# Kernel tuning notes

Hardware: AMD Instinct MI355X
Metric: run time of the kernel (lower is better)

The kernel has to match this reference:

```python
import jax, jax.numpy as jnp
import numpy as np

N_EMBD = 768
N_HEAD = 12
HEAD_DIM = N_EMBD // N_HEAD


def setup_inputs() -> dict:
    key = jax.random.key(0)
    k0, k1, k2, k3, k4 = jax.random.split(key, 5)
    B, T, C = 2, 4096, N_EMBD
    x = jax.random.normal(k0, (B, T, C), dtype=jnp.float32)
    # c_attn: Linear(C, 3C); c_proj: Linear(C, C). torch Linear: y = x @ W.T + b
    s = 1.0 / np.sqrt(C)
    W_attn = jax.random.uniform(k1, (3 * C, C), dtype=jnp.float32, minval=-s, maxval=s)
    b_attn = jax.random.uniform(k2, (3 * C,), dtype=jnp.float32, minval=-s, maxval=s)
    W_proj = jax.random.uniform(k3, (C, C), dtype=jnp.float32, minval=-s, maxval=s)
    b_proj = jax.random.uniform(k4, (C,), dtype=jnp.float32, minval=-s, maxval=s)
    return {"x": x, "W_attn": W_attn, "b_attn": b_attn, "W_proj": W_proj, "b_proj": b_proj}


def reference(x, W_attn, b_attn, W_proj, b_proj):
    B, T, C = x.shape
    H, D = N_HEAD, HEAD_DIM
    qkv = x @ W_attn.T + b_attn                      # [B,T,3C]
    q, k, v = jnp.split(qkv, 3, axis=-1)
    # [B,T,C] -> [B,H,T,D]
    q = q.reshape(B, T, H, D).transpose(0, 2, 1, 3)
    k = k.reshape(B, T, H, D).transpose(0, 2, 1, 3)
    v = v.reshape(B, T, H, D).transpose(0, 2, 1, 3)
    scale = 1.0 / jnp.sqrt(jnp.asarray(D, dtype=x.dtype))
    att = jnp.einsum('bhqd,bhkd->bhqk', q, k) * scale  # [B,H,T,T]
    att = jax.nn.softmax(att, axis=-1)
    y = jnp.einsum('bhqk,bhkd->bhqd', att, v)          # [B,H,T,D]
    y = y.transpose(0, 2, 1, 3).reshape(B, T, C)
    return y @ W_proj.T + b_proj
```

## Files before the change

### kernel.cpp

```cpp
#include <hip/hip_runtime.h>
#include <stdint.h>
#include <stddef.h>

typedef __bf16 bf16_t;
typedef bf16_t bf16x4 __attribute__((ext_vector_type(4)));
typedef bf16_t bf16x8 __attribute__((ext_vector_type(8)));
typedef float  f32x4  __attribute__((ext_vector_type(4)));

#define MFMA16(a, b, c) __builtin_amdgcn_mfma_f32_16x16x32_bf16(a, b, c, 0, 0, 0)

__device__ __forceinline__ void gload_lds16(const bf16_t* g, bf16_t* l) {
    __builtin_amdgcn_global_load_lds(
        (const __attribute__((address_space(1))) void*)g,
        (__attribute__((address_space(3))) void*)l,
        16, 0, 0);
}

__global__ void cvt_f32_bf16(const float* __restrict__ in, bf16_t* __restrict__ out, int n4) {
    int i = blockIdx.x * blockDim.x + threadIdx.x;
    if (i >= n4) return;
    float4 f = ((const float4*)in)[i];
    bf16x4 o = { (bf16_t)f.x, (bf16_t)f.y, (bf16_t)f.z, (bf16_t)f.w };
    ((bf16x4*)out)[i] = o;
}

template <int KDIM>
__device__ __forceinline__ void gemm_mainloop(
    const bf16_t* __restrict__ A, const bf16_t* __restrict__ Bt,
    bf16_t* As, bf16_t* Bs, int m0, int n0, int wave, int lane, f32x4 acc[4][4])
{
    const int quad = lane >> 4, l15 = lane & 15;
    const int wm = ((wave >> 1) << 6), wn = ((wave & 1) << 6);

    const int srow = (wave << 4) + (lane >> 2);
    const int sw   = (((lane & 3) ^ ((srow >> 1) & 3)) << 3);
    const bf16_t* gA = A  + (size_t)(m0 + srow) * KDIM + sw;
    const bf16_t* gB = Bt + (size_t)(n0 + srow) * KDIM + sw;
    bf16_t* lA0 = As + wave * 512;
    bf16_t* lA1 = As + 2048 + wave * 512;
    bf16_t* lB0 = Bs + wave * 512;
    bf16_t* lB1 = Bs + 2048 + wave * 512;

    const int xorv = ((quad ^ ((l15 >> 1) & 3)) << 3);

    for (int k0 = 0; k0 < KDIM; k0 += 32) {
        __syncthreads();
        gload_lds16(gA + k0,                       lA0);
        gload_lds16(gA + (size_t)64 * KDIM + k0,   lA1);
        gload_lds16(gB + k0,                       lB0);
        gload_lds16(gB + (size_t)64 * KDIM + k0,   lB1);
        __syncthreads();

        bf16x8 af[4], bfr[4];
#pragma unroll
        for (int t = 0; t < 4; t++) {
            af[t]  = *(const bf16x8*)(As + (wm + t * 16 + l15) * 32 + xorv);
            bfr[t] = *(const bf16x8*)(Bs + (wn + t * 16 + l15) * 32 + xorv);
        }
#pragma unroll
        for (int mt = 0; mt < 4; mt++)
#pragma unroll
            for (int nt = 0; nt < 4; nt++)
                acc[mt][nt] = MFMA16(af[mt], bfr[nt], acc[mt][nt]);
    }
}

__global__ __launch_bounds__(256) void gemm_qkv(
    const bf16_t* __restrict__ A,
    const bf16_t* __restrict__ Bt,
    const float* __restrict__ bias,
    bf16_t* __restrict__ qo, bf16_t* __restrict__ ko, bf16_t* __restrict__ vo)
{
    __shared__ bf16_t As[128 * 32];
    __shared__ bf16_t Bs[128 * 32];
    const int tid = threadIdx.x, wave = tid >> 6, lane = tid & 63;
    const int quad = lane >> 4, l15 = lane & 15;
    const int m0 = blockIdx.y * 128, n0 = blockIdx.x * 128;
    f32x4 acc[4][4] = {};
    gemm_mainloop<768>(A, Bt, As, Bs, m0, n0, wave, lane, acc);

    const int wm = ((wave >> 1) << 6), wn = ((wave & 1) << 6);
#pragma unroll
    for (int nt = 0; nt < 4; nt++) {
        const int cc = n0 + wn + nt * 16 + l15;
        const float bia = bias[cc];
        const int which = cc / 768;
        const int rem = cc - which * 768;
        const int h = rem >> 6, d = rem & 63;
        if (which < 2) {
            bf16_t* dst = (which == 0) ? qo : ko;
#pragma unroll
            for (int mt = 0; mt < 4; mt++) {
#pragma unroll
                for (int r = 0; r < 4; r++) {
                    const int row = m0 + wm + mt * 16 + quad * 4 + r;
                    const int b = row >> 12, t = row & 4095;
                    dst[((size_t)(b * 12 + h) * 4096 + t) * 64 + d] =
                        (bf16_t)(acc[mt][nt][r] + bia);
                }
            }
        } else {
#pragma unroll
            for (int mt = 0; mt < 4; mt++) {
                const int row0 = m0 + wm + mt * 16 + quad * 4;
                const int b = row0 >> 12, t0 = row0 & 4095;
                bf16x4 ov = { (bf16_t)(acc[mt][nt][0] + bia),
                              (bf16_t)(acc[mt][nt][1] + bia),
                              (bf16_t)(acc[mt][nt][2] + bia),
                              (bf16_t)(acc[mt][nt][3] + bia) };
                *(bf16x4*)(vo + ((size_t)(b * 12 + h) * 64 + d) * 4096 + t0) = ov;
            }
        }
    }
}

__global__ __launch_bounds__(256) void gemm_proj(
    const bf16_t* __restrict__ A,
    const bf16_t* __restrict__ Bt,
    const float* __restrict__ bias,
    float* __restrict__ out)
{
    __shared__ bf16_t As[128 * 32];
    __shared__ bf16_t Bs[128 * 32];
    const int tid = threadIdx.x, wave = tid >> 6, lane = tid & 63;
    const int quad = lane >> 4, l15 = lane & 15;
    const int m0 = blockIdx.y * 128, n0 = blockIdx.x * 128;
    f32x4 acc[4][4] = {};
    gemm_mainloop<768>(A, Bt, As, Bs, m0, n0, wave, lane, acc);

    const int wm = ((wave >> 1) << 6), wn = ((wave & 1) << 6);
#pragma unroll
    for (int nt = 0; nt < 4; nt++) {
        const int cc = n0 + wn + nt * 16 + l15;
        const float bia = bias[cc];
#pragma unroll
        for (int mt = 0; mt < 4; mt++) {
#pragma unroll
            for (int r = 0; r < 4; r++) {
                const int row = m0 + wm + mt * 16 + quad * 4 + r;
                out[(size_t)row * 768 + cc] = acc[mt][nt][r] + bia;
            }
        }
    }
}

#define QSCALE 0.1803368801f
__global__ __launch_bounds__(256, 3) void attn_fwd(
    const bf16_t* __restrict__ qg, const bf16_t* __restrict__ kg,
    const bf16_t* __restrict__ vtg, bf16_t* __restrict__ y)
{
    __shared__ bf16_t Ks0[64 * 64], Ks1[64 * 64];
    __shared__ bf16_t Vt0[64 * 64], Vt1[64 * 64];
    __shared__ bf16_t Ps[4][16 * 72];
    const int tid = threadIdx.x, wave = tid >> 6, lane = tid & 63;
    const int quad = lane >> 4, l15 = lane & 15;
    const int qt = blockIdx.x, bh = blockIdx.y;
    const int b = bh / 12, h = bh - b * 12;
    const size_t base = (size_t)bh * 4096 * 64;
    const bf16_t* kgt = kg + base;
    const bf16_t* vgt = vtg + base;

    bf16x8 qf[2][2];
#pragma unroll
    for (int rt = 0; rt < 2; rt++) {
        const int qrow = qt * 128 + wave * 32 + rt * 16 + l15;
        qf[rt][0] = *(const bf16x8*)(qg + base + (size_t)qrow * 64 + quad * 8);
        qf[rt][1] = *(const bf16x8*)(qg + base + (size_t)qrow * 64 + 32 + quad * 8);
#pragma unroll
        for (int j = 0; j < 8; j++) {
            qf[rt][0][j] = (bf16_t)((float)qf[rt][0][j] * QSCALE);
            qf[rt][1][j] = (bf16_t)((float)qf[rt][1][j] * QSCALE);
        }
    }

    const bf16_t one = (bf16_t)1.0f;
    const bf16x8 ones = { one, one, one, one, one, one, one, one };

    f32x4 O[2][4] = {};
    f32x4 Osum[2] = {};

    const int srow8 = tid >> 3;
    const int sc8   = (tid & 7) ^ (srow8 & 7);
    const int ksoff = (quad ^ (l15 & 7)) << 3;

    auto stage = [&](int kt, bf16_t* Kd, bf16_t* Vd) {
        const bf16_t* kp = kgt + (size_t)kt * 64 * 64;
        const bf16_t* vp = vgt + kt * 64;
#pragma unroll
        for (int i = 0; i < 2; i++) {
            gload_lds16(kp + (i * 32 + srow8) * 64 + sc8 * 8,          Kd + (i * 256 + tid) * 8);
            gload_lds16(vp + (size_t)(i * 32 + srow8) * 4096 + sc8 * 8, Vd + (i * 256 + tid) * 8);
        }
    };

    auto compute = [&](const bf16_t* ks, const bf16_t* vs) {
        f32x4 sc[2][4];
#pragma unroll
        for (int ct = 0; ct < 4; ct++) {
            const bf16_t* kr = ks + (ct * 16 + l15) * 64;
            bf16x8 kf0 = *(const bf16x8*)(kr + ksoff);
            bf16x8 kf1 = *(const bf16x8*)(kr + (ksoff ^ 32));
            f32x4 s0 = {}, s1 = {};
            s0 = MFMA16(qf[0][0], kf0, s0);
            s0 = MFMA16(qf[0][1], kf1, s0);
            s1 = MFMA16(qf[1][0], kf0, s1);
            s1 = MFMA16(qf[1][1], kf1, s1);
            sc[0][ct] = s0; sc[1][ct] = s1;
        }
        bf16x8 pf[2][2];
        bf16_t* pw = &Ps[wave][0];
#pragma unroll
        for (int rt = 0; rt < 2; rt++) {
#pragma unroll
            for (int ct = 0; ct < 4; ct++)
#pragma unroll
                for (int r = 0; r < 4; r++)
                    pw[(quad * 4 + r) * 72 + ct * 16 + l15] =
                        (bf16_t)exp2f(sc[rt][ct][r]);
#pragma unroll
            for (int kk = 0; kk < 2; kk++)
                pf[rt][kk] = *(const bf16x8*)(pw + l15 * 72 + kk * 32 + quad * 8);
        }
#pragma unroll
        for (int dt = 0; dt < 4; dt++) {
            const bf16_t* vr = vs + (dt * 16 + l15) * 64;
#pragma unroll
            for (int kk = 0; kk < 2; kk++) {
                bf16x8 vf = *(const bf16x8*)(vr + (ksoff ^ (kk << 5)));
                O[0][dt] = MFMA16(pf[0][kk], vf, O[0][dt]);
                O[1][dt] = MFMA16(pf[1][kk], vf, O[1][dt]);
            }
        }
#pragma unroll
        for (int rt = 0; rt < 2; rt++)
#pragma unroll
            for (int kk = 0; kk < 2; kk++)
                Osum[rt] = MFMA16(pf[rt][kk], ones, Osum[rt]);
    };

    stage(0, Ks0, Vt0);
    for (int kt = 0; kt < 64; kt += 2) {
        __syncthreads();
        stage(kt + 1, Ks1, Vt1);
        compute(Ks0, Vt0);
        __syncthreads();
        if (kt + 2 < 64) stage(kt + 2, Ks0, Vt0);
        compute(Ks1, Vt1);
    }

#pragma unroll
    for (int rt = 0; rt < 2; rt++) {
        float rcp[4];
#pragma unroll
        for (int r = 0; r < 4; r++) rcp[r] = 1.0f / Osum[rt][r];
#pragma unroll
        for (int dt = 0; dt < 4; dt++)
#pragma unroll
            for (int r = 0; r < 4; r++) {
                const int t = qt * 128 + wave * 32 + rt * 16 + quad * 4 + r;
                const int c = h * 64 + dt * 16 + l15;
                y[((size_t)b * 4096 + t) * 768 + c] = (bf16_t)(O[rt][dt][r] * rcp[r]);
            }
    }
}

extern "C" void kernel_launch(void* const* d_in, const int* in_sizes, int n_in,
                              void* d_out, int out_size, void* d_ws, size_t ws_size,
                              hipStream_t stream) {
    const float* x  = (const float*)d_in[0];
    const float* Wa = (const float*)d_in[1];
    const float* ba = (const float*)d_in[2];
    const float* Wp = (const float*)d_in[3];
    const float* bp = (const float*)d_in[4];
    float* out = (float*)d_out;

    char* ws = (char*)d_ws;
    bf16_t* xb  = (bf16_t*)(ws);
    bf16_t* Wab = (bf16_t*)(ws + 12582912);
    bf16_t* Wpb = (bf16_t*)(ws + 16121856);
    bf16_t* qb  = (bf16_t*)(ws + 17301504);
    bf16_t* kb  = (bf16_t*)(ws + 29884416);
    bf16_t* vtb = (bf16_t*)(ws + 42467328);
    bf16_t* yb  = (bf16_t*)(ws + 55050240);

    cvt_f32_bf16<<<6144, 256, 0, stream>>>(x,  xb,  1572864);
    cvt_f32_bf16<<<1728, 256, 0, stream>>>(Wa, Wab,  442368);
    cvt_f32_bf16<<< 576, 256, 0, stream>>>(Wp, Wpb,  147456);

    gemm_qkv <<<dim3(18, 64), 256, 0, stream>>>(xb, Wab, ba, qb, kb, vtb);
    attn_fwd <<<dim3(32, 24), 256, 0, stream>>>(qb, kb, vtb, yb);
    gemm_proj<<<dim3( 6, 64), 256, 0, stream>>>(yb, Wpb, bp, out);
}
```

Measured before the change: 314.6 us.

## Keep attention probabilities in registers via transposed QK MFMA and fp16 PV

```diff
diff --git a/kernel.cpp b/kernel.cpp
--- a/kernel.cpp
+++ b/kernel.cpp
@@ -6,22 +6,33 @@
 typedef bf16_t bf16x4 __attribute__((ext_vector_type(4)));
 typedef bf16_t bf16x8 __attribute__((ext_vector_type(8)));
 typedef float  f32x4  __attribute__((ext_vector_type(4)));
-
-#define MFMA16(a, b, c) __builtin_amdgcn_mfma_f32_16x16x32_bf16(a, b, c, 0, 0, 0)
-
-__device__ __forceinline__ void gload_lds16(const bf16_t* g, bf16_t* l) {
+typedef _Float16 f16_t;
+typedef f16_t f16x4 __attribute__((ext_vector_type(4)));
+
+#define MFMA_BF16_K32(a, b, c) __builtin_amdgcn_mfma_f32_16x16x32_bf16(a, b, c, 0, 0, 0)
+#define MFMA_F16_K16(a, b, c)  __builtin_amdgcn_mfma_f32_16x16x16f16(a, b, c, 0, 0, 0)
+
+__device__ __forceinline__ void gload_lds16(const void* g, void* l) {
     __builtin_amdgcn_global_load_lds(
         (const __attribute__((address_space(1))) void*)g,
         (__attribute__((address_space(3))) void*)l,
         16, 0, 0);
 }
 
-__global__ void cvt_f32_bf16(const float* __restrict__ in, bf16_t* __restrict__ out, int n4) {
+#define NX 1572864
+#define NWA 442368
+#define NWP 147456
+__global__ void cvt_all(const float* __restrict__ x, const float* __restrict__ Wa,
+                        const float* __restrict__ Wp, bf16_t* __restrict__ xb,
+                        bf16_t* __restrict__ Wab, bf16_t* __restrict__ Wpb) {
     int i = blockIdx.x * blockDim.x + threadIdx.x;
-    if (i >= n4) return;
-    float4 f = ((const float4*)in)[i];
+    const float4* src; bf16_t* dst; int j;
+    if (i < NX)            { src = (const float4*)x;  dst = xb;  j = i; }
+    else if (i < NX + NWA) { src = (const float4*)Wa; dst = Wab; j = i - NX; }
+    else                   { src = (const float4*)Wp; dst = Wpb; j = i - NX - NWA; }
+    float4 f = src[j];
     bf16x4 o = { (bf16_t)f.x, (bf16_t)f.y, (bf16_t)f.z, (bf16_t)f.w };
-    ((bf16x4*)out)[i] = o;
+    ((bf16x4*)dst)[j] = o;
 }
 
 template <int KDIM>
@@ -61,7 +72,7 @@
         for (int mt = 0; mt < 4; mt++)
 #pragma unroll
             for (int nt = 0; nt < 4; nt++)
-                acc[mt][nt] = MFMA16(af[mt], bfr[nt], acc[mt][nt]);
+                acc[mt][nt] = MFMA_BF16_K32(af[mt], bfr[nt], acc[mt][nt]);
     }
 }
 
@@ -69,7 +80,7 @@
     const bf16_t* __restrict__ A,
     const bf16_t* __restrict__ Bt,
     const float* __restrict__ bias,
-    bf16_t* __restrict__ qo, bf16_t* __restrict__ ko, bf16_t* __restrict__ vo)
+    bf16_t* __restrict__ qo, bf16_t* __restrict__ ko, f16_t* __restrict__ vo)
 {
     __shared__ bf16_t As[128 * 32];
     __shared__ bf16_t Bs[128 * 32];
@@ -104,11 +115,11 @@
             for (int mt = 0; mt < 4; mt++) {
                 const int row0 = m0 + wm + mt * 16 + quad * 4;
                 const int b = row0 >> 12, t0 = row0 & 4095;
-                bf16x4 ov = { (bf16_t)(acc[mt][nt][0] + bia),
-                              (bf16_t)(acc[mt][nt][1] + bia),
-                              (bf16_t)(acc[mt][nt][2] + bia),
-                              (bf16_t)(acc[mt][nt][3] + bia) };
-                *(bf16x4*)(vo + ((size_t)(b * 12 + h) * 64 + d) * 4096 + t0) = ov;
+                f16x4 ov = { (f16_t)(acc[mt][nt][0] + bia),
+                             (f16_t)(acc[mt][nt][1] + bia),
+                             (f16_t)(acc[mt][nt][2] + bia),
+                             (f16_t)(acc[mt][nt][3] + bia) };
+                *(f16x4*)(vo + ((size_t)(b * 12 + h) * 64 + d) * 4096 + t0) = ov;
             }
         }
     }
@@ -147,18 +158,17 @@
 #define QSCALE 0.1803368801f
 __global__ __launch_bounds__(256, 3) void attn_fwd(
     const bf16_t* __restrict__ qg, const bf16_t* __restrict__ kg,
-    const bf16_t* __restrict__ vtg, bf16_t* __restrict__ y)
+    const f16_t* __restrict__ vtg, bf16_t* __restrict__ y)
 {
     __shared__ bf16_t Ks0[64 * 64], Ks1[64 * 64];
-    __shared__ bf16_t Vt0[64 * 64], Vt1[64 * 64];
-    __shared__ bf16_t Ps[4][16 * 72];
+    __shared__ f16_t  Vt0[64 * 64], Vt1[64 * 64];
     const int tid = threadIdx.x, wave = tid >> 6, lane = tid & 63;
     const int quad = lane >> 4, l15 = lane & 15;
     const int qt = blockIdx.x, bh = blockIdx.y;
     const int b = bh / 12, h = bh - b * 12;
     const size_t base = (size_t)bh * 4096 * 64;
     const bf16_t* kgt = kg + base;
-    const bf16_t* vgt = vtg + base;
+    const f16_t*  vgt = vtg + base;
 
     bf16x8 qf[2][2];
 #pragma unroll
@@ -173,8 +183,8 @@
         }
     }
 
-    const bf16_t one = (bf16_t)1.0f;
-    const bf16x8 ones = { one, one, one, one, one, one, one, one };
+    const f16_t onef = (f16_t)1.0f;
+    const f16x4 onesf = { onef, onef, onef, onef };
 
     f32x4 O[2][4] = {};
     f32x4 Osum[2] = {};
@@ -182,18 +192,19 @@
     const int srow8 = tid >> 3;
     const int sc8   = (tid & 7) ^ (srow8 & 7);
     const int ksoff = (quad ^ (l15 & 7)) << 3;
-
-    auto stage = [&](int kt, bf16_t* Kd, bf16_t* Vd) {
+    const int l8 = l15 & 7, q1 = quad >> 1, q0off = (quad & 1) * 8;
+
+    auto stage = [&](int kt, bf16_t* Kd, f16_t* Vd) {
         const bf16_t* kp = kgt + (size_t)kt * 64 * 64;
-        const bf16_t* vp = vgt + kt * 64;
+        const f16_t*  vp = vgt + kt * 64;
 #pragma unroll
         for (int i = 0; i < 2; i++) {
-            gload_lds16(kp + (i * 32 + srow8) * 64 + sc8 * 8,          Kd + (i * 256 + tid) * 8);
+            gload_lds16(kp + (i * 32 + srow8) * 64 + sc8 * 8,           Kd + (i * 256 + tid) * 8);
             gload_lds16(vp + (size_t)(i * 32 + srow8) * 4096 + sc8 * 8, Vd + (i * 256 + tid) * 8);
         }
     };
 
-    auto compute = [&](const bf16_t* ks, const bf16_t* vs) {
+    auto compute = [&](const bf16_t* ks, const f16_t* vs) {
         f32x4 sc[2][4];
 #pragma unroll
         for (int ct = 0; ct < 4; ct++) {
@@ -201,41 +212,37 @@
             bf16x8 kf0 = *(const bf16x8*)(kr + ksoff);
             bf16x8 kf1 = *(const bf16x8*)(kr + (ksoff ^ 32));
             f32x4 s0 = {}, s1 = {};
-            s0 = MFMA16(qf[0][0], kf0, s0);
-            s0 = MFMA16(qf[0][1], kf1, s0);
-            s1 = MFMA16(qf[1][0], kf0, s1);
-            s1 = MFMA16(qf[1][1], kf1, s1);
+            s0 = MFMA_BF16_K32(kf0, qf[0][0], s0);
+            s0 = MFMA_BF16_K32(kf1, qf[0][1], s0);
+            s1 = MFMA_BF16_K32(kf0, qf[1][0], s1);
+            s1 = MFMA_BF16_K32(kf1, qf[1][1], s1);
             sc[0][ct] = s0; sc[1][ct] = s1;
         }
-        bf16x8 pf[2][2];
-        bf16_t* pw = &Ps[wave][0];
-#pragma unroll
-        for (int rt = 0; rt < 2; rt++) {
-#pragma unroll
-            for (int ct = 0; ct < 4; ct++)
-#pragma unroll
-                for (int r = 0; r < 4; r++)
-                    pw[(quad * 4 + r) * 72 + ct * 16 + l15] =
-                        (bf16_t)exp2f(sc[rt][ct][r]);
-#pragma unroll
-            for (int kk = 0; kk < 2; kk++)
-                pf[rt][kk] = *(const bf16x8*)(pw + l15 * 72 + kk * 32 + quad * 8);
-        }
+        f16x4 pf[2][4];
+#pragma unroll
+        for (int rt = 0; rt < 2; rt++)
+#pragma unroll
+            for (int ct = 0; ct < 4; ct++) {
+                f16x4 p = { (f16_t)exp2f(sc[rt][ct][0]), (f16_t)exp2f(sc[rt][ct][1]),
+                            (f16_t)exp2f(sc[rt][ct][2]), (f16_t)exp2f(sc[rt][ct][3]) };
+                pf[rt][ct] = p;
+            }
 #pragma unroll
         for (int dt = 0; dt < 4; dt++) {
-            const bf16_t* vr = vs + (dt * 16 + l15) * 64;
-#pragma unroll
-            for (int kk = 0; kk < 2; kk++) {
-                bf16x8 vf = *(const bf16x8*)(vr + (ksoff ^ (kk << 5)));
-                O[0][dt] = MFMA16(pf[0][kk], vf, O[0][dt]);
-                O[1][dt] = MFMA16(pf[1][kk], vf, O[1][dt]);
+            const char* vr = (const char*)(vs + (dt * 16 + l15) * 64);
+#pragma unroll
+            for (int kk = 0; kk < 4; kk++) {
+                const int slot = ((kk << 1) | q1) ^ l8;
+                f16x4 vf = *(const f16x4*)(vr + slot * 16 + q0off);
+                O[0][dt] = MFMA_F16_K16(vf, pf[0][kk], O[0][dt]);
+                O[1][dt] = MFMA_F16_K16(vf, pf[1][kk], O[1][dt]);
             }
         }
 #pragma unroll
         for (int rt = 0; rt < 2; rt++)
 #pragma unroll
-            for (int kk = 0; kk < 2; kk++)
-                Osum[rt] = MFMA16(pf[rt][kk], ones, Osum[rt]);
+            for (int kk = 0; kk < 4; kk++)
+                Osum[rt] = MFMA_F16_K16(onesf, pf[rt][kk], Osum[rt]);
     };
 
     stage(0, Ks0, Vt0);
@@ -250,17 +257,15 @@
 
 #pragma unroll
     for (int rt = 0; rt < 2; rt++) {
-        float rcp[4];
-#pragma unroll
-        for (int r = 0; r < 4; r++) rcp[r] = 1.0f / Osum[rt][r];
-#pragma unroll
-        for (int dt = 0; dt < 4; dt++)
-#pragma unroll
-            for (int r = 0; r < 4; r++) {
-                const int t = qt * 128 + wave * 32 + rt * 16 + quad * 4 + r;
-                const int c = h * 64 + dt * 16 + l15;
-                y[((size_t)b * 4096 + t) * 768 + c] = (bf16_t)(O[rt][dt][r] * rcp[r]);
-            }
+        const float rcp = 1.0f / Osum[rt][0];
+        const int t = qt * 128 + wave * 32 + rt * 16 + l15;
+        bf16_t* yr = y + ((size_t)b * 4096 + t) * 768 + h * 64 + quad * 4;
+#pragma unroll
+        for (int dt = 0; dt < 4; dt++) {
+            bf16x4 ov = { (bf16_t)(O[rt][dt][0] * rcp), (bf16_t)(O[rt][dt][1] * rcp),
+                          (bf16_t)(O[rt][dt][2] * rcp), (bf16_t)(O[rt][dt][3] * rcp) };
+            *(bf16x4*)(yr + dt * 16) = ov;
+        }
     }
 }
 
@@ -280,13 +285,10 @@
     bf16_t* Wpb = (bf16_t*)(ws + 16121856);
     bf16_t* qb  = (bf16_t*)(ws + 17301504);
     bf16_t* kb  = (bf16_t*)(ws + 29884416);
-    bf16_t* vtb = (bf16_t*)(ws + 42467328);
+    f16_t*  vtb = (f16_t*)(ws + 42467328);
     bf16_t* yb  = (bf16_t*)(ws + 55050240);
 
-    cvt_f32_bf16<<<6144, 256, 0, stream>>>(x,  xb,  1572864);
-    cvt_f32_bf16<<<1728, 256, 0, stream>>>(Wa, Wab,  442368);
-    cvt_f32_bf16<<< 576, 256, 0, stream>>>(Wp, Wpb,  147456);
-
+    cvt_all<<<8448, 256, 0, stream>>>(x, Wa, Wp, xb, Wab, Wpb);
     gemm_qkv <<<dim3(18, 64), 256, 0, stream>>>(xb, Wab, ba, qb, kb, vtb);
     attn_fwd <<<dim3(32, 24), 256, 0, stream>>>(qb, kb, vtb, yb);
     gemm_proj<<<dim3( 6, 64), 256, 0, stream>>>(yb, Wpb, bp, out);
```

New measurement: 313.2 us. About the same (-0.4%).
